# Performance work log

Hardware: AMD Instinct MI355X
Metric: run time of the kernel (lower is better)

Reference implementation:

```python
import jax, jax.numpy as jnp
import numpy as np

N_NODES = 100000
N_EDGES = 1600000
IN_DIM = 256
OUT_DIM = 128


def setup_inputs() -> dict:
    key = jax.random.key(0)
    k1, k2, k3, k4, k5, k6 = jax.random.split(key, 6)
    H = jax.random.normal(k1, (N_NODES, IN_DIM), dtype=jnp.float32)
    std = 1.0 / np.sqrt(OUT_DIM)
    weight = jax.random.uniform(k2, (IN_DIM, OUT_DIM), dtype=jnp.float32, minval=-std, maxval=std)
    bias = jax.random.uniform(k3, (OUT_DIM,), dtype=jnp.float32, minval=-std, maxval=std)
    # COO representation of the normalized sparse adjacency A [N, N]
    src = jax.random.randint(k4, (N_EDGES,), 0, N_NODES, dtype=jnp.int32)
    dst = jnp.sort(jax.random.randint(k5, (N_EDGES,), 0, N_NODES, dtype=jnp.int32))
    vals = jax.random.uniform(k6, (N_EDGES,), dtype=jnp.float32) / 16.0  # ~row-normalized
    return {"H": H, "weight": weight, "bias": bias, "vals": vals, "src": src, "dst": dst}


def reference(H, weight, bias, vals, src, dst):
    # Dense transform: [N, K] @ [K, D] -> [N, D]
    HW = H @ weight
    # SpMM (A @ HW) as gather-scale-scatter over COO edges
    msg = HW[src] * vals[:, None]                      # [E, D]
    out = jax.ops.segment_sum(msg, dst, num_segments=H.shape[0])
    return out + bias
```

## Files before the change

kernel.cpp:

```cpp
#include <hip/hip_runtime.h>
#include <hip/hip_bf16.h>

#define N_NODES 100000
#define N_EDGES 1600000
#define IN_DIM 256
#define OUT_DIM 128

typedef __attribute__((ext_vector_type(4))) float f32x4;
typedef __attribute__((ext_vector_type(8))) short s16x8;

__device__ inline unsigned short f2bf_us(float f) {
    union { __hip_bfloat16 h; unsigned short u; } v;
    v.h = __float2bfloat16(f);
    return v.u;
}

__device__ inline s16x8 pack8(const float4& a, const float4& b) {
    union { s16x8 v; __hip_bfloat162 h[4]; } u;
    u.h[0] = __float22bfloat162_rn(make_float2(a.x, a.y));
    u.h[1] = __float22bfloat162_rn(make_float2(a.z, a.w));
    u.h[2] = __float22bfloat162_rn(make_float2(b.x, b.y));
    u.h[3] = __float22bfloat162_rn(make_float2(b.z, b.w));
    return u.v;
}

__device__ inline void gload_lds16(const float* g, float* l) {
    __builtin_amdgcn_global_load_lds(
        (const __attribute__((address_space(1))) unsigned*)g,
        (__attribute__((address_space(3))) unsigned*)l, 16, 0, 0);
}

__global__ __launch_bounds__(256)
void wt_kernel(const float* __restrict__ W, unsigned short* __restrict__ WTx) {
    const int t = blockIdx.x * 256 + threadIdx.x;
    const int j    = t & 7;
    const int lrow = (t >> 3) & 15;
    const int kblk = (t >> 7) & 3;
    const int kc   = (t >> 9) & 7;
    const int n    = t >> 12;
    const int k    = kc * 32 + kblk * 8 + j;
    const int c    = n * 16 + lrow;
    WTx[t] = f2bf_us(W[(size_t)k * OUT_DIM + c]);
}

__global__ __launch_bounds__(256, 3)
void gemm_mfma_kernel(const float* __restrict__ H,
                      const unsigned short* __restrict__ WTx,
                      unsigned short* __restrict__ HWp) {
    __shared__ float Hs[2][4096];

    const int tid  = threadIdx.x;
    const int wid  = tid >> 6;
    const int lane = tid & 63;
    const int lrow = lane & 15;
    const int kblk = lane >> 4;
    const int brow = blockIdx.x * 128;

    const unsigned short* wbase = WTx + (size_t)(kblk * 16 + lrow) * 8;

    f32x4 acc[2][8] = {};

    auto stage = [&](int b, int kc) {
        #pragma unroll
        for (int i = 0; i < 4; ++i) {
            const int ubase = i * 256 + wid * 64;
            const int unit  = ubase + lane;
            const int row   = unit >> 3;
            const int ul    = (unit & 7) ^ (row & 7);
            int grow = brow + row; if (grow >= N_NODES) grow = N_NODES - 1;
            const float* gsrc = H + (size_t)grow * IN_DIM + kc * 32 + ul * 4;
            gload_lds16(gsrc, &Hs[b][ubase * 4]);
        }
    };

    stage(0, 0);
    __syncthreads();

    for (int kc = 0; kc < 8; ++kc) {
        const int cur = kc & 1;
        if (kc < 7) stage(cur ^ 1, kc + 1);

        s16x8 fa[2];
        #pragma unroll
        for (int mt = 0; mt < 2; ++mt) {
            const int row = wid * 32 + mt * 16 + lrow;
            const int u0  = (kblk * 2) ^ (row & 7);
            const int u1  = (kblk * 2 + 1) ^ (row & 7);
            const float4 x0 = *(const float4*)&Hs[cur][(row * 8 + u0) * 4];
            const float4 x1 = *(const float4*)&Hs[cur][(row * 8 + u1) * 4];
            fa[mt] = pack8(x0, x1);
        }
        #pragma unroll
        for (int n = 0; n < 8; ++n) {
            const s16x8 fb = *(const s16x8*)(wbase + ((size_t)(n * 8 + kc) << 9));
            acc[0][n] = __builtin_amdgcn_mfma_f32_16x16x32_bf16(fa[0], fb, acc[0][n], 0, 0, 0);
            acc[1][n] = __builtin_amdgcn_mfma_f32_16x16x32_bf16(fa[1], fb, acc[1][n], 0, 0, 0);
        }
        __syncthreads();
    }

    const int c = lane & 15;
    #pragma unroll
    for (int mt = 0; mt < 2; ++mt) {
        #pragma unroll
        for (int r = 0; r < 4; ++r) {
            const int grow = brow + wid * 32 + mt * 16 + (lane >> 4) * 4 + r;
            if (grow < N_NODES) {
                unsigned short tmp[8];
                #pragma unroll
                for (int n = 0; n < 8; ++n) tmp[n] = f2bf_us(acc[mt][n][r]);
                *(s16x8*)(HWp + (size_t)grow * OUT_DIM + c * 8) = *(const s16x8*)tmp;
            }
        }
    }
}

__global__ __launch_bounds__(256)
void rowptr_kernel(const int* __restrict__ dst, int* __restrict__ row_ptr) {
    const int e = blockIdx.x * blockDim.x + threadIdx.x;
    if (e > N_EDGES) return;
    if (e == N_EDGES) {
        for (int n = dst[N_EDGES - 1] + 1; n <= N_NODES; ++n) row_ptr[n] = N_EDGES;
        return;
    }
    const int d = dst[e];
    const int dprev = (e == 0) ? -1 : dst[e - 1];
    for (int n = dprev + 1; n <= d; ++n) row_ptr[n] = e;
}

__global__ __launch_bounds__(256)
void spmm_v3_kernel(const uint4* __restrict__ HWq, const float* __restrict__ vals,
                    const int* __restrict__ src, const int* __restrict__ row_ptr,
                    const float* __restrict__ bias, float* __restrict__ out) {
    const int node = blockIdx.x * 4 + (threadIdx.x >> 6);
    if (node >= N_NODES) return;
    const int lane  = threadIdx.x & 63;
    const int eslot = lane >> 4;
    const int cg    = lane & 15;

    const int lo = row_ptr[node];
    const int hi = row_ptr[node + 1];

    float acc[8] = {};
    for (int base = lo; base < hi; base += 8) {
        const int e0 = base + eslot;
        const int e1 = base + 4 + eslot;
        const bool m0 = e0 < hi;
        const bool m1 = e1 < hi;
        const int ec0 = m0 ? e0 : lo;
        const int ec1 = m1 ? e1 : lo;
        const int   s0 = src[ec0];
        const int   s1 = src[ec1];
        const float v0 = m0 ? vals[ec0] : 0.f;
        const float v1 = m1 ? vals[ec1] : 0.f;
        const uint4 g0 = HWq[(size_t)s0 * 16 + cg];
        const uint4 g1 = HWq[(size_t)s1 * 16 + cg];

        const unsigned* u0 = (const unsigned*)&g0;
        const unsigned* u1 = (const unsigned*)&g1;
        #pragma unroll
        for (int j = 0; j < 4; ++j) {
            acc[2*j]   = fmaf(__uint_as_float(u0[j] << 16),         v0, acc[2*j]);
            acc[2*j+1] = fmaf(__uint_as_float(u0[j] & 0xffff0000u), v0, acc[2*j+1]);
        }
        #pragma unroll
        for (int j = 0; j < 4; ++j) {
            acc[2*j]   = fmaf(__uint_as_float(u1[j] << 16),         v1, acc[2*j]);
            acc[2*j+1] = fmaf(__uint_as_float(u1[j] & 0xffff0000u), v1, acc[2*j+1]);
        }
    }

    #pragma unroll
    for (int i = 0; i < 8; ++i) {
        acc[i] += __shfl_xor(acc[i], 16);
        acc[i] += __shfl_xor(acc[i], 32);
    }

    if (lane < 16) {
        #pragma unroll
        for (int j = 0; j < 8; ++j)
            out[(size_t)node * OUT_DIM + j * 16 + cg] = acc[j] + bias[j * 16 + cg];
    }
}

extern "C" void kernel_launch(void* const* d_in, const int* in_sizes, int n_in,
                              void* d_out, int out_size, void* d_ws, size_t ws_size,
                              hipStream_t stream) {
    const float* H    = (const float*)d_in[0];
    const float* W    = (const float*)d_in[1];
    const float* bias = (const float*)d_in[2];
    const float* vals = (const float*)d_in[3];
    const int*   src  = (const int*)d_in[4];
    const int*   dst  = (const int*)d_in[5];
    float* out = (float*)d_out;

    unsigned short* HWp = (unsigned short*)d_ws;
    const size_t hw_bytes = (size_t)N_NODES * OUT_DIM * sizeof(unsigned short);
    int* row_ptr = (int*)((char*)d_ws + hw_bytes);
    size_t wt_off = hw_bytes + (size_t)(N_NODES + 1) * sizeof(int);
    wt_off = (wt_off + 127) & ~(size_t)127;
    unsigned short* WTx = (unsigned short*)((char*)d_ws + wt_off);

    wt_kernel<<<dim3((IN_DIM * OUT_DIM) / 256), dim3(256), 0, stream>>>(W, WTx);
    rowptr_kernel<<<dim3((N_EDGES + 256) / 256), dim3(256), 0, stream>>>(dst, row_ptr);
    gemm_mfma_kernel<<<dim3((N_NODES + 127) / 128), dim3(256), 0, stream>>>(H, WTx, HWp);
    spmm_v3_kernel<<<dim3((N_NODES + 3) / 4), dim3(256), 0, stream>>>(
        (const uint4*)HWp, vals, src, row_ptr, bias, out);
}
```

Measured before the change: 105.4 us.

## Split HW into eight column slabs and make SpMM gather per slab

The GEMM epilogue now writes HW as eight column slabs of 16 bf16 each, node-major within a slab. The SpMM launches eight times as many blocks, one per (node group, slab), so each lane gathers 4 bytes from a 3.2 MB slab instead of 16 bytes from the full 25.6 MB matrix. The goal is for the working set of each slab's random gathers to fit in cache. In exchange, src and vals are read eight times (with nontemporal hints), the GEMM epilogue uses scattered 2-byte stores, and the gathers become narrower.

```diff
diff --git a/kernel.cpp b/kernel.cpp
--- a/kernel.cpp
+++ b/kernel.cpp
@@ -46,7 +46,7 @@
 __global__ __launch_bounds__(256, 3)
 void gemm_mfma_kernel(const float* __restrict__ H,
                       const unsigned short* __restrict__ WTx,
-                      unsigned short* __restrict__ HWp) {
+                      unsigned short* __restrict__ HWs) {
     __shared__ float Hs[2][4096];
 
     const int tid  = threadIdx.x;
@@ -106,10 +106,10 @@
         for (int r = 0; r < 4; ++r) {
             const int grow = brow + wid * 32 + mt * 16 + (lane >> 4) * 4 + r;
             if (grow < N_NODES) {
-                unsigned short tmp[8];
                 #pragma unroll
-                for (int n = 0; n < 8; ++n) tmp[n] = f2bf_us(acc[mt][n][r]);
-                *(s16x8*)(HWp + (size_t)grow * OUT_DIM + c * 8) = *(const s16x8*)tmp;
+                for (int n = 0; n < 8; ++n)
+                    HWs[(size_t)n * (N_NODES * 16) + (size_t)grow * 16 + c] =
+                        f2bf_us(acc[mt][n][r]);
             }
         }
     }
@@ -129,57 +129,51 @@
 }
 
 __global__ __launch_bounds__(256)
-void spmm_v3_kernel(const uint4* __restrict__ HWq, const float* __restrict__ vals,
-                    const int* __restrict__ src, const int* __restrict__ row_ptr,
-                    const float* __restrict__ bias, float* __restrict__ out) {
-    const int node = blockIdx.x * 4 + (threadIdx.x >> 6);
+void spmm_v5_kernel(const unsigned int* __restrict__ HWsu,
+                    const float* __restrict__ vals,
+                    const int* __restrict__ src,
+                    const int* __restrict__ row_ptr,
+                    const float* __restrict__ bias,
+                    float* __restrict__ out) {
+    const int p    = blockIdx.x & 7;
+    const int node = (blockIdx.x >> 3) * 4 + (threadIdx.x >> 6);
     if (node >= N_NODES) return;
     const int lane  = threadIdx.x & 63;
-    const int eslot = lane >> 4;
-    const int cg    = lane & 15;
+    const int eslot = lane >> 3;
+    const int cg    = lane & 7;
+
+    const unsigned int* __restrict__ slab = HWsu + (size_t)p * (N_NODES * 8);
 
     const int lo = row_ptr[node];
     const int hi = row_ptr[node + 1];
 
-    float acc[8] = {};
-    for (int base = lo; base < hi; base += 8) {
+    float ax = 0.f, ay = 0.f;
+    for (int base = lo; base < hi; base += 16) {
         const int e0 = base + eslot;
-        const int e1 = base + 4 + eslot;
-        const bool m0 = e0 < hi;
-        const bool m1 = e1 < hi;
+        const int e1 = base + 8 + eslot;
+        const bool m0 = e0 < hi, m1 = e1 < hi;
         const int ec0 = m0 ? e0 : lo;
         const int ec1 = m1 ? e1 : lo;
-        const int   s0 = src[ec0];
-        const int   s1 = src[ec1];
-        const float v0 = m0 ? vals[ec0] : 0.f;
-        const float v1 = m1 ? vals[ec1] : 0.f;
-        const uint4 g0 = HWq[(size_t)s0 * 16 + cg];
-        const uint4 g1 = HWq[(size_t)s1 * 16 + cg];
-
-        const unsigned* u0 = (const unsigned*)&g0;
-        const unsigned* u1 = (const unsigned*)&g1;
-        #pragma unroll
-        for (int j = 0; j < 4; ++j) {
-            acc[2*j]   = fmaf(__uint_as_float(u0[j] << 16),         v0, acc[2*j]);
-            acc[2*j+1] = fmaf(__uint_as_float(u0[j] & 0xffff0000u), v0, acc[2*j+1]);
-        }
-        #pragma unroll
-        for (int j = 0; j < 4; ++j) {
-            acc[2*j]   = fmaf(__uint_as_float(u1[j] << 16),         v1, acc[2*j]);
-            acc[2*j+1] = fmaf(__uint_as_float(u1[j] & 0xffff0000u), v1, acc[2*j+1]);
-        }
-    }
-
-    #pragma unroll
-    for (int i = 0; i < 8; ++i) {
-        acc[i] += __shfl_xor(acc[i], 16);
-        acc[i] += __shfl_xor(acc[i], 32);
-    }
-
-    if (lane < 16) {
-        #pragma unroll
-        for (int j = 0; j < 8; ++j)
-            out[(size_t)node * OUT_DIM + j * 16 + cg] = acc[j] + bias[j * 16 + cg];
+        const int   s0 = __builtin_nontemporal_load(&src[ec0]);
+        const int   s1 = __builtin_nontemporal_load(&src[ec1]);
+        const float v0 = m0 ? __builtin_nontemporal_load(&vals[ec0]) : 0.f;
+        const float v1 = m1 ? __builtin_nontemporal_load(&vals[ec1]) : 0.f;
+        const unsigned u0 = slab[(size_t)s0 * 8 + cg];
+        const unsigned u1 = slab[(size_t)s1 * 8 + cg];
+        ax = fmaf(__uint_as_float(u0 << 16),         v0, ax);
+        ay = fmaf(__uint_as_float(u0 & 0xffff0000u), v0, ay);
+        ax = fmaf(__uint_as_float(u1 << 16),         v1, ax);
+        ay = fmaf(__uint_as_float(u1 & 0xffff0000u), v1, ay);
+    }
+
+    ax += __shfl_xor(ax, 8);  ay += __shfl_xor(ay, 8);
+    ax += __shfl_xor(ax, 16); ay += __shfl_xor(ay, 16);
+    ax += __shfl_xor(ax, 32); ay += __shfl_xor(ay, 32);
+
+    if (lane < 8) {
+        const int c = p * 16 + cg * 2;
+        __builtin_nontemporal_store(ax + bias[c],     &out[(size_t)node * OUT_DIM + c]);
+        __builtin_nontemporal_store(ay + bias[c + 1], &out[(size_t)node * OUT_DIM + c + 1]);
     }
 }
 
@@ -194,7 +188,7 @@
     const int*   dst  = (const int*)d_in[5];
     float* out = (float*)d_out;
 
-    unsigned short* HWp = (unsigned short*)d_ws;
+    unsigned short* HWs = (unsigned short*)d_ws;
     const size_t hw_bytes = (size_t)N_NODES * OUT_DIM * sizeof(unsigned short);
     int* row_ptr = (int*)((char*)d_ws + hw_bytes);
     size_t wt_off = hw_bytes + (size_t)(N_NODES + 1) * sizeof(int);
@@ -203,7 +197,9 @@
 
     wt_kernel<<<dim3((IN_DIM * OUT_DIM) / 256), dim3(256), 0, stream>>>(W, WTx);
     rowptr_kernel<<<dim3((N_EDGES + 256) / 256), dim3(256), 0, stream>>>(dst, row_ptr);
-    gemm_mfma_kernel<<<dim3((N_NODES + 127) / 128), dim3(256), 0, stream>>>(H, WTx, HWp);
-    spmm_v3_kernel<<<dim3((N_NODES + 3) / 4), dim3(256), 0, stream>>>(
-        (const uint4*)HWp, vals, src, row_ptr, bias, out);
-}
+    gemm_mfma_kernel<<<dim3((N_NODES + 127) / 128), dim3(256), 0, stream>>>(H, WTx, HWs);
+
+    const int node_blocks = (N_NODES + 3) / 4;
+    spmm_v5_kernel<<<dim3(node_blocks * 8), dim3(256), 0, stream>>>(
+        (const unsigned int*)HWs, vals, src, row_ptr, bias, out);
+}
```

After: 317.6 us. 3.01x slower.
